# Optimization experiments

Measured on AMD Instinct MI355X. Metric: run time of the kernel, lower is better.

Reference implementation:

```python
import jax, jax.numpy as jnp
import numpy as np

B, S, D, H = 8, 1024, 768, 12
HD = D // H  # head_dim = 64


def setup_inputs() -> dict:
    key = jax.random.key(0)
    ks = jax.random.split(key, 9)
    s = 0.02
    return {
        "hidden_states": jax.random.normal(ks[0], (B, S, D), dtype=jnp.float32),
        "Wq": jax.random.normal(ks[1], (D, D), dtype=jnp.float32) * s,
        "bq": jnp.zeros((D,), dtype=jnp.float32),
        "Wk": jax.random.normal(ks[2], (D, D), dtype=jnp.float32) * s,
        "bk": jnp.zeros((D,), dtype=jnp.float32),
        "Wv": jax.random.normal(ks[3], (D, D), dtype=jnp.float32) * s,
        "bv": jnp.zeros((D,), dtype=jnp.float32),
        "Wo": jax.random.normal(ks[4], (D, D), dtype=jnp.float32) * s,
        "bo": jnp.zeros((D,), dtype=jnp.float32),
    }


def reference(hidden_states, Wq, bq, Wk, bk, Wv, bv, Wo, bo):
    b, s, d = hidden_states.shape
    scale = 1.0 / jnp.sqrt(jnp.asarray(HD, dtype=hidden_states.dtype))
    # projections (weights stored as [in, out])
    q = hidden_states @ Wq + bq
    k = hidden_states @ Wk + bk
    v = hidden_states @ Wv + bv
    # [B, H, S, HD]
    q = q.reshape(b, s, H, HD).transpose(0, 2, 1, 3)
    k = k.reshape(b, s, H, HD).transpose(0, 2, 1, 3)
    v = v.reshape(b, s, H, HD).transpose(0, 2, 1, 3)
    # explicit O(S^2) attention, matching the original unfused math
    attn = jnp.einsum("bhqd,bhkd->bhqk", q, k) * scale
    attn = jax.nn.softmax(attn, axis=-1)
    out = jnp.einsum("bhqk,bhkd->bhqd", attn, v)
    out = out.transpose(0, 2, 1, 3).reshape(b, s, d)
    return out @ Wo + bo
```

## Files before the change

kernel.cpp:

```cpp
#include <hip/hip_runtime.h>
#include <stdint.h>

#define DEV __device__ __forceinline__

typedef __attribute__((ext_vector_type(8))) short bf16x8;
typedef __attribute__((ext_vector_type(4))) float f32x4;

#define MFMA16(a,b,c) __builtin_amdgcn_mfma_f32_16x16x32_bf16((a),(b),(c),0,0,0)

#define GL_LDS(SRC, DST) \
  __builtin_amdgcn_global_load_lds( \
      (const __attribute__((address_space(1))) void*)(SRC), \
      (__attribute__((address_space(3))) void*)(DST), 16, 0, 0)

DEV unsigned short f2bf(float x){
  union { float f; unsigned u; } v; v.f = x;
  unsigned r = v.u + 0x7fffu + ((v.u >> 16) & 1u);
  return (unsigned short)(r >> 16);
}
DEV unsigned pack2(float a, float b){
  return (unsigned)f2bf(a) | ((unsigned)f2bf(b) << 16);
}
DEV bf16x8 mk_bf16x8(unsigned w0, unsigned w1, unsigned w2, unsigned w3){
  union { uint4 u; bf16x8 v; } cv;
  cv.u = make_uint4(w0, w1, w2, w3);
  return cv.v;
}
DEV void bar(){
  asm volatile("" ::: "memory");
  __builtin_amdgcn_s_barrier();
  asm volatile("" ::: "memory");
}

__global__ void cast_x_kernel(const float* __restrict__ x, uint4* __restrict__ out){
  int i = blockIdx.x * 256 + threadIdx.x;
  const float4* p = (const float4*)x + (size_t)i * 2;
  float4 a = p[0], b = p[1];
  out[i] = make_uint4(pack2(a.x,a.y), pack2(a.z,a.w), pack2(b.x,b.y), pack2(b.z,b.w));
}

__global__ void trans_w_kernel(const float* __restrict__ W0, const float* __restrict__ W1,
                               const float* __restrict__ W2, const float* __restrict__ W3,
                               unsigned short* __restrict__ T0, unsigned short* __restrict__ T1,
                               unsigned short* __restrict__ T2, unsigned short* __restrict__ T3){
  const float* W; unsigned short* T;
  switch (blockIdx.z) {
    case 0:  W = W0; T = T0; break;
    case 1:  W = W1; T = T1; break;
    case 2:  W = W2; T = T2; break;
    default: W = W3; T = T3; break;
  }
  __shared__ float tile[32][33];
  const int i0 = blockIdx.y * 32, o0 = blockIdx.x * 32;
  const int t = threadIdx.x;
  const int ir = t >> 3, oc = (t & 7) * 4;
  float4 v = *(const float4*)(W + (size_t)(i0 + ir) * 768 + o0 + oc);
  tile[ir][oc+0] = v.x; tile[ir][oc+1] = v.y; tile[ir][oc+2] = v.z; tile[ir][oc+3] = v.w;
  __syncthreads();
  const int orow = t >> 3, ic = (t & 7) * 4;
  uint2 w;
  w.x = pack2(tile[ic+0][orow], tile[ic+1][orow]);
  w.y = pack2(tile[ic+2][orow], tile[ic+3][orow]);
  *(uint2*)(T + (size_t)(o0 + orow) * 768 + i0 + ic) = w;
}

__launch_bounds__(512, 2)
__global__ void gemm_qkv(const unsigned short* __restrict__ Wcat,
                         const unsigned short* __restrict__ X16,
                         const float* __restrict__ bq, const float* __restrict__ bk,
                         const float* __restrict__ bv,
                         unsigned short* __restrict__ Qb, unsigned short* __restrict__ Kb,
                         unsigned short* __restrict__ VTb)
{
  __shared__ __align__(16) unsigned char lds[2][2][2][16384];
  const int tid = threadIdx.x;
  const int lane = tid & 63, wid = tid >> 6;
  const int lin = blockIdx.x;
  const int nid = (lin & 7) * 36 + (lin >> 3);
  const int m0 = (nid % 9) * 256;
  const int n0 = (nid / 9) * 256;
  const int wm = wid >> 2, wn = wid & 3;

  const int c1 = tid,       r1 = ((c1 >> 6) << 4) + (c1 & 15), kg1 = (c1 >> 4) & 3;
  const int c2 = 512 + tid, r2 = ((c2 >> 6) << 4) + (c2 & 15), kg2 = (c2 >> 4) & 3;
  const unsigned short* Abase = Wcat + (size_t)m0 * 768;
  const unsigned short* Bbase = X16  + (size_t)n0 * 768;

  #define STAGE(TILE, AB, KK) do {                                              \
    const unsigned short* sb_ = (AB) ? Bbase : Abase;                           \
    const int ko_ = (TILE) * 64 + (KK) * 32;                                    \
    GL_LDS(sb_ + (size_t)r1 * 768 + ko_ + kg1 * 8, &lds[(TILE)&1][AB][KK][c1*16]); \
    GL_LDS(sb_ + (size_t)r2 * 768 + ko_ + kg2 * 8, &lds[(TILE)&1][AB][KK][c2*16]); \
  } while (0)

  #define PHASE(BUF, KK, NH, STAGE_STMT)                                        \
  {                                                                             \
    if ((NH) == 0) {                                                            \
      _Pragma("unroll")                                                         \
      for (int mb = 0; mb < 8; ++mb)                                            \
        afr[mb] = *(const bf16x8*)&lds[BUF][0][KK][((wm*8+mb)*64 + lane)*16];   \
    }                                                                           \
    bf16x8 bfr0 = *(const bf16x8*)&lds[BUF][1][KK][((wn*4+(NH)*2+0)*64+lane)*16]; \
    bf16x8 bfr1 = *(const bf16x8*)&lds[BUF][1][KK][((wn*4+(NH)*2+1)*64+lane)*16]; \
    STAGE_STMT;                                                                 \
    bar();                                                                      \
    __builtin_amdgcn_s_setprio(1);                                              \
    _Pragma("unroll")                                                           \
    for (int mb = 0; mb < 8; ++mb) {                                            \
      acc[mb][(NH)*2+0] = MFMA16(afr[mb], bfr0, acc[mb][(NH)*2+0]);             \
      acc[mb][(NH)*2+1] = MFMA16(afr[mb], bfr1, acc[mb][(NH)*2+1]);             \
    }                                                                           \
    __builtin_amdgcn_s_setprio(0);                                              \
    asm volatile("s_waitcnt vmcnt(8)" ::: "memory");                            \
    bar();                                                                      \
  }

  f32x4 acc[8][4] = {};
  bf16x8 afr[8];

  STAGE(0, 0, 0);
  STAGE(0, 1, 0);
  STAGE(0, 0, 1);
  STAGE(0, 1, 1);
  STAGE(1, 0, 0);
  STAGE(1, 1, 0);
  asm volatile("s_waitcnt vmcnt(8)" ::: "memory");
  bar();

  for (int i = 0; i < 6; ++i) {
    const int k0t = 2 * i, k1t = 2 * i + 1;
    const bool pf = (i < 5);
    PHASE(0, 0, 0, { STAGE(k1t, 0, 1); })
    PHASE(0, 0, 1, { STAGE(k1t, 1, 1); })
    PHASE(0, 1, 0, { if (pf) STAGE(k0t + 2, 0, 0); })
    PHASE(0, 1, 1, { if (pf) STAGE(k0t + 2, 1, 0); })
    PHASE(1, 0, 0, { if (pf) STAGE(k0t + 2, 0, 1); })
    PHASE(1, 0, 1, { if (pf) STAGE(k0t + 2, 1, 1); })
    PHASE(1, 1, 0, { if (pf) STAGE(k1t + 2, 0, 0); })
    PHASE(1, 1, 1, { if (pf) STAGE(k1t + 2, 1, 0); })
  }
  #undef PHASE
  #undef STAGE

  const int l15 = lane & 15, lg = lane >> 4;
  const int sel = m0 / 768;
  const int mbase = m0 - sel * 768;
  #pragma unroll
  for (int mb = 0; mb < 8; ++mb) {
    #pragma unroll
    for (int nb = 0; nb < 4; ++nb) {
      const int rowl = wm * 128 + mb * 16 + lg * 4;
      const int coll = wn * 64 + nb * 16 + l15;
      f32x4 a = acc[mb][nb];
      const int chan = mbase + rowl;
      const int sg   = n0 + coll;
      const int b = sg >> 10, s = sg & 1023, h = chan >> 6, hd = chan & 63;
      if (sel != 2) {
        float4 bi = *(const float4*)((sel == 0 ? bq : bk) + chan);
        uint2 w;
        w.x = pack2(a[0] + bi.x, a[1] + bi.y);
        w.y = pack2(a[2] + bi.z, a[3] + bi.w);
        unsigned short* o = (sel == 0 ? Qb : Kb);
        *(uint2*)(o + ((size_t)(b * 12 + h) * 1024 + s) * 64 + hd) = w;
      } else {
        float4 bi = *(const float4*)(bv + chan);
        size_t base = ((size_t)(b * 12 + h) * 64 + hd) * 1024 + s;
        VTb[base       ] = f2bf(a[0] + bi.x);
        VTb[base + 1024] = f2bf(a[1] + bi.y);
        VTb[base + 2048] = f2bf(a[2] + bi.z);
        VTb[base + 3072] = f2bf(a[3] + bi.w);
      }
    }
  }
}

__launch_bounds__(256, 3)
__global__ void gemm_out(const unsigned short* __restrict__ matA,
                         const unsigned short* __restrict__ matB,
                         float* __restrict__ outp,
                         const float* __restrict__ bias)
{
  __shared__ __align__(16) unsigned char ldsA[2][4096];
  __shared__ __align__(16) unsigned char ldsB[2][8192];
  const int lane = threadIdx.x & 63, wid = threadIdx.x >> 6;
  const int lin = blockIdx.x;
  const int nid = (lin & 7) * 96 + (lin >> 3);
  const int m0 = (nid % 12) * 64;
  const int n0 = (nid / 12) * 128;
  const int wm = wid >> 1, wn = wid & 1;

  f32x4 acc[2][4] = {};

  for (int t = 0; t < 24; ++t) {
    const int buf = t & 1;
    const int k0 = t * 32;
    {
      const int c   = wid * 64 + lane;
      const int row = ((c >> 6) << 4) + (c & 15);
      const int kk  = ((c >> 4) & 3) * 8;
      const unsigned short* sa = matA + (size_t)(m0 + row) * 768 + k0 + kk;
      GL_LDS(sa, &ldsA[buf][c * 16]);
    }
    #pragma unroll
    for (int i = 0; i < 2; ++i) {
      const int c   = i * 256 + wid * 64 + lane;
      const int row = ((c >> 6) << 4) + (c & 15);
      const int kk  = ((c >> 4) & 3) * 8;
      const unsigned short* sb = matB + (size_t)(n0 + row) * 768 + k0 + kk;
      GL_LDS(sb, &ldsB[buf][c * 16]);
    }
    __syncthreads();

    bf16x8 afr[2], bfr[4];
    #pragma unroll
    for (int mb = 0; mb < 2; ++mb)
      afr[mb] = *(const bf16x8*)&ldsA[buf][((wm * 2 + mb) * 64 + lane) * 16];
    #pragma unroll
    for (int nb = 0; nb < 4; ++nb)
      bfr[nb] = *(const bf16x8*)&ldsB[buf][((wn * 4 + nb) * 64 + lane) * 16];
    #pragma unroll
    for (int mb = 0; mb < 2; ++mb)
      #pragma unroll
      for (int nb = 0; nb < 4; ++nb)
        acc[mb][nb] = MFMA16(afr[mb], bfr[nb], acc[mb][nb]);
  }

  const int l15 = lane & 15, lg = lane >> 4;
  #pragma unroll
  for (int mb = 0; mb < 2; ++mb) {
    #pragma unroll
    for (int nb = 0; nb < 4; ++nb) {
      const int rowl = wm * 32 + mb * 16 + lg * 4;
      const int coll = wn * 64 + nb * 16 + l15;
      f32x4 a = acc[mb][nb];
      int chan = m0 + rowl, sg = n0 + coll;
      float4 bi = *(const float4*)(bias + chan);
      float4 o = make_float4(a[0] + bi.x, a[1] + bi.y, a[2] + bi.z, a[3] + bi.w);
      *(float4*)(outp + (size_t)sg * 768 + chan) = o;
    }
  }
}

__launch_bounds__(256, 4)
__global__ void attn_kernel(const unsigned short* __restrict__ Q,
                            const unsigned short* __restrict__ K,
                            const unsigned short* __restrict__ VT,
                            unsigned short* __restrict__ AO)
{
  __shared__ __align__(16) unsigned char kbuf[8192];
  __shared__ __align__(16) unsigned char vbuf[8192];
  const int lane = threadIdx.x & 63, wid = threadIdx.x >> 6;
  const int l15 = lane & 15, lg = lane >> 4;
  const int bh = blockIdx.x;
  const int q0 = blockIdx.y * 128 + wid * 32;
  const unsigned short* Qp = Q  + (size_t)bh * 65536;
  const unsigned short* Kp = K  + (size_t)bh * 65536;
  const unsigned short* Vp = VT + (size_t)bh * 65536;

  bf16x8 qf[2][2];
  #pragma unroll
  for (int f = 0; f < 2; ++f)
    #pragma unroll
    for (int kc = 0; kc < 2; ++kc)
      qf[f][kc] = *(const bf16x8*)(Qp + (size_t)(q0 + f * 16 + l15) * 64 + kc * 32 + lg * 8);

  f32x4 acco[2][4] = {};
  float lsum[2] = {0.f, 0.f};

  const int src0 = l15 + ((lg & 1) << 5);
  const int src1 = src0 + 16;
  const bool hi = (lg & 2) != 0;

  for (int t = 0; t < 16; ++t) {
    const int kv0 = t * 64;
    #pragma unroll
    for (int i = 0; i < 2; ++i) {
      const int g = wid * 2 + i;
      const unsigned short* sk = Kp + (size_t)(kv0 + (g >> 1) * 16 + l15) * 64 + (g & 1) * 32 + lg * 8;
      GL_LDS(sk, &kbuf[g * 1024]);
      const unsigned short* sv = Vp + (size_t)((g >> 1) * 16 + l15) * 1024 + kv0 + (g & 1) * 32 + lg * 8;
      GL_LDS(sv, &vbuf[g * 1024]);
    }
    __syncthreads();

    f32x4 sc[2][4] = {};
    #pragma unroll
    for (int mb = 0; mb < 4; ++mb) {
      #pragma unroll
      for (int kc = 0; kc < 2; ++kc) {
        bf16x8 kf = *(const bf16x8*)&kbuf[((mb * 2 + kc) * 64 + lane) * 16];
        sc[0][mb] = MFMA16(kf, qf[0][kc], sc[0][mb]);
        sc[1][mb] = MFMA16(kf, qf[1][kc], sc[1][mb]);
      }
    }
    unsigned p01[2][4], p23[2][4];
    #pragma unroll
    for (int f = 0; f < 2; ++f) {
      float sum = 0.f;
      #pragma unroll
      for (int mb = 0; mb < 4; ++mb) {
        float e0 = __expf(sc[f][mb][0] * 0.125f);
        float e1 = __expf(sc[f][mb][1] * 0.125f);
        float e2 = __expf(sc[f][mb][2] * 0.125f);
        float e3 = __expf(sc[f][mb][3] * 0.125f);
        sum += (e0 + e1) + (e2 + e3);
        p01[f][mb] = pack2(e0, e1);
        p23[f][mb] = pack2(e2, e3);
      }
      sum += __shfl_xor(sum, 16);
      sum += __shfl_xor(sum, 32);
      lsum[f] += sum;
    }
    bf16x8 pf[2][2];
    #pragma unroll
    for (int f = 0; f < 2; ++f) {
      #pragma unroll
      for (int c = 0; c < 2; ++c) {
        unsigned a0 = __shfl(p01[f][2*c], src0), b0 = __shfl(p01[f][2*c+1], src0);
        unsigned a1 = __shfl(p23[f][2*c], src0), b1 = __shfl(p23[f][2*c+1], src0);
        unsigned a2 = __shfl(p01[f][2*c], src1), b2 = __shfl(p01[f][2*c+1], src1);
        unsigned a3 = __shfl(p23[f][2*c], src1), b3 = __shfl(p23[f][2*c+1], src1);
        pf[f][c] = mk_bf16x8(hi ? b0 : a0, hi ? b1 : a1, hi ? b2 : a2, hi ? b3 : a3);
      }
    }
    #pragma unroll
    for (int hb = 0; hb < 4; ++hb) {
      #pragma unroll
      for (int c = 0; c < 2; ++c) {
        bf16x8 vf = *(const bf16x8*)&vbuf[((hb * 2 + c) * 64 + lane) * 16];
        acco[0][hb] = MFMA16(vf, pf[0][c], acco[0][hb]);
        acco[1][hb] = MFMA16(vf, pf[1][c], acco[1][hb]);
      }
    }
    __syncthreads();
  }

  const int b = bh / 12, h = bh % 12;
  #pragma unroll
  for (int f = 0; f < 2; ++f) {
    const float rl = 1.0f / lsum[f];
    const int s = q0 + f * 16 + l15;
    const size_t base = ((size_t)(b * 1024 + s)) * 768 + h * 64;
    #pragma unroll
    for (int hb = 0; hb < 4; ++hb) {
      uint2 w;
      w.x = pack2(acco[f][hb][0] * rl, acco[f][hb][1] * rl);
      w.y = pack2(acco[f][hb][2] * rl, acco[f][hb][3] * rl);
      *(uint2*)(AO + base + hb * 16 + lg * 4) = w;
    }
  }
}

extern "C" void kernel_launch(void* const* d_in, const int* in_sizes, int n_in,
                              void* d_out, int out_size, void* d_ws, size_t ws_size,
                              hipStream_t stream)
{
  const float* hs = (const float*)d_in[0];
  const float* Wq = (const float*)d_in[1];
  const float* bq = (const float*)d_in[2];
  const float* Wk = (const float*)d_in[3];
  const float* bk = (const float*)d_in[4];
  const float* Wv = (const float*)d_in[5];
  const float* bv = (const float*)d_in[6];
  const float* Wo = (const float*)d_in[7];
  const float* bo = (const float*)d_in[8];

  const size_t SZ_X = (size_t)8192 * 768 * 2;
  const size_t SZ_W = (size_t)768 * 768 * 2;
  const size_t NEED = SZ_X * 5 + SZ_W * 4;
  if (ws_size < NEED) return;

  char* ws = (char*)d_ws;
  unsigned short* X16 = (unsigned short*)ws;
  unsigned short* Wqt = (unsigned short*)(ws + SZ_X);
  unsigned short* Wkt = Wqt + 768 * 768;
  unsigned short* Wvt = Wkt + 768 * 768;
  unsigned short* Wot = Wvt + 768 * 768;
  unsigned short* Qb  = (unsigned short*)(ws + SZ_X + 4 * SZ_W);
  unsigned short* Kb  = Qb  + (size_t)8192 * 768;
  unsigned short* VTb = Kb  + (size_t)8192 * 768;
  unsigned short* AOb = VTb + (size_t)8192 * 768;

  cast_x_kernel<<<dim3(3072), dim3(256), 0, stream>>>(hs, (uint4*)X16);
  trans_w_kernel<<<dim3(24, 24, 4), dim3(256), 0, stream>>>(Wq, Wk, Wv, Wo, Wqt, Wkt, Wvt, Wot);

  gemm_qkv<<<dim3(288), dim3(512), 0, stream>>>(Wqt, X16, bq, bk, bv, Qb, Kb, VTb);

  attn_kernel<<<dim3(96, 8), dim3(256), 0, stream>>>(Qb, Kb, VTb, AOb);

  gemm_out<<<dim3(768), dim3(256), 0, stream>>>(Wot, AOb, (float*)d_out, bo);
}
```

Measured before the change: 162.5 us.

## Retile QKV GEMM to 288x256 tiles so the grid is exactly 256 blocks

The QKV projection GEMM now uses 288-row weight tiles (9 MFMA row blocks per wave) instead of 256, giving 8x32 = 256 workgroups instead of 288. This matches one wave of blocks to the 256 CUs of the MI355X and removes the tail of a second partial wave. A-fragments are now read from LDS inside the MFMA loop instead of being cached in registers, which adds LDS traffic but reduces register pressure from the larger accumulator. The staging uses a third partial load and a new vmcnt threshold. The epilogue computes Q/K/V selection per row block, because a tile can now straddle the Q/K/V boundaries.

```diff
diff --git a/kernel.cpp b/kernel.cpp
--- a/kernel.cpp
+++ b/kernel.cpp
@@ -72,89 +72,93 @@
                          unsigned short* __restrict__ Qb, unsigned short* __restrict__ Kb,
                          unsigned short* __restrict__ VTb)
 {
-  __shared__ __align__(16) unsigned char lds[2][2][2][16384];
+  __shared__ __align__(16) unsigned char a_lds[2][2][18432];
+  __shared__ __align__(16) unsigned char b_lds[2][2][16384];
   const int tid = threadIdx.x;
-  const int lane = tid & 63, wid = tid >> 6;
+  const int lane = tid & 63;
+  const int wid = tid >> 6;
   const int lin = blockIdx.x;
-  const int nid = (lin & 7) * 36 + (lin >> 3);
-  const int m0 = (nid % 9) * 256;
-  const int n0 = (nid / 9) * 256;
+  const int nid = (lin & 7) * 32 + (lin >> 3);
+  const int m0 = (nid & 7) * 288;
+  const int n0 = (nid >> 3) * 256;
   const int wm = wid >> 2, wn = wid & 3;
 
-  const int c1 = tid,       r1 = ((c1 >> 6) << 4) + (c1 & 15), kg1 = (c1 >> 4) & 3;
-  const int c2 = 512 + tid, r2 = ((c2 >> 6) << 4) + (c2 & 15), kg2 = (c2 >> 4) & 3;
+  const int c1 = tid,               r1 = ((c1 >> 6) << 4) + (c1 & 15), kg1 = (c1 >> 4) & 3;
+  const int c2 = 512 + tid,         r2 = ((c2 >> 6) << 4) + (c2 & 15), kg2 = (c2 >> 4) & 3;
+  const int c3 = 1024 + (tid & 127),r3 = ((c3 >> 6) << 4) + (c3 & 15), kg3 = (c3 >> 4) & 3;
   const unsigned short* Abase = Wcat + (size_t)m0 * 768;
   const unsigned short* Bbase = X16  + (size_t)n0 * 768;
 
-  #define STAGE(TILE, AB, KK) do {                                              \
-    const unsigned short* sb_ = (AB) ? Bbase : Abase;                           \
-    const int ko_ = (TILE) * 64 + (KK) * 32;                                    \
-    GL_LDS(sb_ + (size_t)r1 * 768 + ko_ + kg1 * 8, &lds[(TILE)&1][AB][KK][c1*16]); \
-    GL_LDS(sb_ + (size_t)r2 * 768 + ko_ + kg2 * 8, &lds[(TILE)&1][AB][KK][c2*16]); \
+  #define STAGE_A(TILE, KK) do {                                                   \
+    const int ko_ = (TILE) * 64 + (KK) * 32;                                       \
+    GL_LDS(Abase + (size_t)r1 * 768 + ko_ + kg1 * 8, &a_lds[(TILE)&1][KK][c1*16]); \
+    GL_LDS(Abase + (size_t)r2 * 768 + ko_ + kg2 * 8, &a_lds[(TILE)&1][KK][c2*16]); \
+    GL_LDS(Abase + (size_t)r3 * 768 + ko_ + kg3 * 8, &a_lds[(TILE)&1][KK][c3*16]); \
   } while (0)
-
-  #define PHASE(BUF, KK, NH, STAGE_STMT)                                        \
-  {                                                                             \
-    if ((NH) == 0) {                                                            \
-      _Pragma("unroll")                                                         \
-      for (int mb = 0; mb < 8; ++mb)                                            \
-        afr[mb] = *(const bf16x8*)&lds[BUF][0][KK][((wm*8+mb)*64 + lane)*16];   \
-    }                                                                           \
-    bf16x8 bfr0 = *(const bf16x8*)&lds[BUF][1][KK][((wn*4+(NH)*2+0)*64+lane)*16]; \
-    bf16x8 bfr1 = *(const bf16x8*)&lds[BUF][1][KK][((wn*4+(NH)*2+1)*64+lane)*16]; \
-    STAGE_STMT;                                                                 \
-    bar();                                                                      \
-    __builtin_amdgcn_s_setprio(1);                                              \
-    _Pragma("unroll")                                                           \
-    for (int mb = 0; mb < 8; ++mb) {                                            \
-      acc[mb][(NH)*2+0] = MFMA16(afr[mb], bfr0, acc[mb][(NH)*2+0]);             \
-      acc[mb][(NH)*2+1] = MFMA16(afr[mb], bfr1, acc[mb][(NH)*2+1]);             \
-    }                                                                           \
-    __builtin_amdgcn_s_setprio(0);                                              \
-    asm volatile("s_waitcnt vmcnt(8)" ::: "memory");                            \
-    bar();                                                                      \
-  }
-
-  f32x4 acc[8][4] = {};
-  bf16x8 afr[8];
-
-  STAGE(0, 0, 0);
-  STAGE(0, 1, 0);
-  STAGE(0, 0, 1);
-  STAGE(0, 1, 1);
-  STAGE(1, 0, 0);
-  STAGE(1, 1, 0);
-  asm volatile("s_waitcnt vmcnt(8)" ::: "memory");
+  #define STAGE_B(TILE, KK) do {                                                   \
+    const int ko_ = (TILE) * 64 + (KK) * 32;                                       \
+    GL_LDS(Bbase + (size_t)r1 * 768 + ko_ + kg1 * 8, &b_lds[(TILE)&1][KK][c1*16]); \
+    GL_LDS(Bbase + (size_t)r2 * 768 + ko_ + kg2 * 8, &b_lds[(TILE)&1][KK][c2*16]); \
+  } while (0)
+
+  #define PHASE(BUF, KK, NH, STAGE_STMT)                                           \
+  {                                                                                \
+    bf16x8 bfr0 = *(const bf16x8*)&b_lds[BUF][KK][((wn*4+(NH)*2+0)*64+lane)*16];   \
+    bf16x8 bfr1 = *(const bf16x8*)&b_lds[BUF][KK][((wn*4+(NH)*2+1)*64+lane)*16];   \
+    STAGE_STMT;                                                                    \
+    bar();                                                                         \
+    __builtin_amdgcn_s_setprio(1);                                                 \
+    _Pragma("unroll")                                                              \
+    for (int mb = 0; mb < 9; ++mb) {                                               \
+      bf16x8 af = *(const bf16x8*)&a_lds[BUF][KK][((wm*9+mb)*64+lane)*16];         \
+      acc[mb][(NH)*2+0] = MFMA16(af, bfr0, acc[mb][(NH)*2+0]);                     \
+      acc[mb][(NH)*2+1] = MFMA16(af, bfr1, acc[mb][(NH)*2+1]);                     \
+    }                                                                              \
+    __builtin_amdgcn_s_setprio(0);                                                 \
+    asm volatile("s_waitcnt vmcnt(10)" ::: "memory");                              \
+    bar();                                                                         \
+  }
+
+  f32x4 acc[9][4] = {};
+
+  STAGE_A(0, 0);
+  STAGE_B(0, 0);
+  STAGE_A(0, 1);
+  STAGE_B(0, 1);
+  STAGE_A(1, 0);
+  STAGE_B(1, 0);
+  asm volatile("s_waitcnt vmcnt(10)" ::: "memory");
   bar();
 
   for (int i = 0; i < 6; ++i) {
     const int k0t = 2 * i, k1t = 2 * i + 1;
     const bool pf = (i < 5);
-    PHASE(0, 0, 0, { STAGE(k1t, 0, 1); })
-    PHASE(0, 0, 1, { STAGE(k1t, 1, 1); })
-    PHASE(0, 1, 0, { if (pf) STAGE(k0t + 2, 0, 0); })
-    PHASE(0, 1, 1, { if (pf) STAGE(k0t + 2, 1, 0); })
-    PHASE(1, 0, 0, { if (pf) STAGE(k0t + 2, 0, 1); })
-    PHASE(1, 0, 1, { if (pf) STAGE(k0t + 2, 1, 1); })
-    PHASE(1, 1, 0, { if (pf) STAGE(k1t + 2, 0, 0); })
-    PHASE(1, 1, 1, { if (pf) STAGE(k1t + 2, 1, 0); })
+    PHASE(0, 0, 0, { STAGE_A(k1t, 1); })
+    PHASE(0, 0, 1, { STAGE_B(k1t, 1); })
+    PHASE(0, 1, 0, { if (pf) STAGE_A(k0t + 2, 0); })
+    PHASE(0, 1, 1, { if (pf) STAGE_B(k0t + 2, 0); })
+    PHASE(1, 0, 0, { if (pf) STAGE_A(k0t + 2, 1); })
+    PHASE(1, 0, 1, { if (pf) STAGE_B(k0t + 2, 1); })
+    PHASE(1, 1, 0, { if (pf) STAGE_A(k1t + 2, 0); })
+    PHASE(1, 1, 1, { if (pf) STAGE_B(k1t + 2, 0); })
   }
   #undef PHASE
-  #undef STAGE
+  #undef STAGE_A
+  #undef STAGE_B
 
   const int l15 = lane & 15, lg = lane >> 4;
-  const int sel = m0 / 768;
-  const int mbase = m0 - sel * 768;
   #pragma unroll
-  for (int mb = 0; mb < 8; ++mb) {
+  for (int mb = 0; mb < 9; ++mb) {
+    const int chan_g = m0 + wm * 144 + mb * 16 + lg * 4;
+    const int sel  = chan_g / 768;
+    const int chan = chan_g - sel * 768;
+    const int h = chan >> 6, hd = chan & 63;
     #pragma unroll
     for (int nb = 0; nb < 4; ++nb) {
-      const int rowl = wm * 128 + mb * 16 + lg * 4;
       const int coll = wn * 64 + nb * 16 + l15;
+      const int sg   = n0 + coll;
+      const int b = sg >> 10, s = sg & 1023;
       f32x4 a = acc[mb][nb];
-      const int chan = mbase + rowl;
-      const int sg   = n0 + coll;
-      const int b = sg >> 10, s = sg & 1023, h = chan >> 6, hd = chan & 63;
       if (sel != 2) {
         float4 bi = *(const float4*)((sel == 0 ? bq : bk) + chan);
         uint2 w;
@@ -384,7 +388,7 @@
   cast_x_kernel<<<dim3(3072), dim3(256), 0, stream>>>(hs, (uint4*)X16);
   trans_w_kernel<<<dim3(24, 24, 4), dim3(256), 0, stream>>>(Wq, Wk, Wv, Wo, Wqt, Wkt, Wvt, Wot);
 
-  gemm_qkv<<<dim3(288), dim3(512), 0, stream>>>(Wqt, X16, bq, bk, bv, Qb, Kb, VTb);
+  gemm_qkv<<<dim3(256), dim3(512), 0, stream>>>(Wqt, X16, bq, bk, bv, Qb, Kb, VTb);
 
   attn_kernel<<<dim3(96, 8), dim3(256), 0, stream>>>(Qb, Kb, VTb, AOb);
 
```

After: 148.6 us. 8.6% less time.
